# Optimization experiments

Hardware: AMD Instinct MI355X
Metric: run time of the kernel (lower is better)

## Reference

```python
import jax, jax.numpy as jnp
import numpy as np

K_TOKENS = 40  # safety_token_count
LN_EPS = 1e-5


def setup_inputs() -> dict:
    key = jax.random.key(0)
    ks = jax.random.split(key, 3)
    B, S, D = 16, 4096, 768
    H = D // 2
    features = jax.random.normal(ks[0], (B, S, D), dtype=jnp.float32)
    W1 = jax.random.normal(ks[1], (D, H), dtype=jnp.float32) * (1.0 / np.sqrt(D))
    b1 = jnp.zeros((H,), dtype=jnp.float32)
    ln_gamma = jnp.ones((H,), dtype=jnp.float32)
    ln_beta = jnp.zeros((H,), dtype=jnp.float32)
    W2 = jax.random.normal(ks[2], (H, 1), dtype=jnp.float32) * (1.0 / np.sqrt(H))
    b2 = jnp.zeros((1,), dtype=jnp.float32)
    return {"features": features, "W1": W1, "b1": b1,
            "ln_gamma": ln_gamma, "ln_beta": ln_beta, "W2": W2, "b2": b2}


def _scores(features, W1, b1, ln_gamma, ln_beta, W2, b2):
    # Linear -> LayerNorm -> GELU(exact) -> Dropout(eval=identity) -> Linear -> Sigmoid
    h = jnp.einsum('bsd,dh->bsh', features, W1) + b1
    mu = jnp.mean(h, axis=-1, keepdims=True)
    var = jnp.mean(jnp.square(h - mu), axis=-1, keepdims=True)
    h = (h - mu) * jax.lax.rsqrt(var + LN_EPS) * ln_gamma + ln_beta
    h = jax.nn.gelu(h, approximate=False)
    s = jnp.einsum('bsh,ho->bso', h, W2) + b2  # [B, S, 1]
    return jax.nn.sigmoid(s[..., 0])           # [B, S]


def reference(features, W1, b1, ln_gamma, ln_beta, W2, b2):
    scores = _scores(features, W1, b1, ln_gamma, ln_beta, W2, b2)
    k = min(K_TOKENS, features.shape[1])
    _, indices = jax.lax.top_k(scores, k)                      # [B, k]
    safety_tokens = jnp.take_along_axis(features, indices[:, :, None], axis=1)  # [B, k, D]
    return safety_tokens, indices
```

## Files before the change

kernel.cpp:

```cpp
#include <hip/hip_runtime.h>
#include <math.h>

#define B_   16
#define S_   4096
#define D_   768
#define H_   384
#define NTOK (B_ * S_)
#define KTOP 40
#define NTILES 24
#define KCH    24

typedef __attribute__((ext_vector_type(8))) short bf16x8;
typedef __attribute__((ext_vector_type(4))) float f32x4;

static __device__ __forceinline__ unsigned short f2bf(float x) {
    union { float f; unsigned u; } v; v.f = x;
    unsigned r = v.u + 0x7FFF + ((v.u >> 16) & 1);
    return (unsigned short)(r >> 16);
}
static __device__ __forceinline__ float bf2f(unsigned short h) {
    union { unsigned u; float f; } v; v.u = ((unsigned)h) << 16; return v.f;
}

__global__ __launch_bounds__(64) void pack_w1(const float* __restrict__ W1,
                                              unsigned short* __restrict__ bh,
                                              unsigned short* __restrict__ bl)
{
    const int nt   = blockIdx.x;
    const int ch   = blockIdx.y;
    const int lane = threadIdx.x;
    const int n    = nt * 16 + (lane & 15);
    const int k0   = ch * 32 + (lane >> 4) * 8;

    unsigned short h8[8], l8[8];
#pragma unroll
    for (int j = 0; j < 8; ++j) {
        const float v = W1[(size_t)(k0 + j) * H_ + n];
        const unsigned short h = f2bf(v);
        h8[j] = h;
        l8[j] = f2bf(v - bf2f(h));
    }
    const size_t base = ((size_t)(nt * KCH + ch) * 64 + lane) * 8;
#pragma unroll
    for (int j = 0; j < 8; ++j) { bh[base + j] = h8[j]; bl[base + j] = l8[j]; }
}

__global__ __launch_bounds__(256, 3) void score_kernel(
    const float* __restrict__ features,
    const unsigned short* __restrict__ bh_g,
    const unsigned short* __restrict__ bl_g,
    const float* __restrict__ b1,
    const float* __restrict__ gamma,
    const float* __restrict__ beta,
    const float* __restrict__ W2,
    const float* __restrict__ b2,
    float* __restrict__ scores)
{
    __shared__ unsigned short Ah[32][40];
    __shared__ unsigned short Al[32][40];
    __shared__ float red[4][32];
    __shared__ float mu_s[32];
    __shared__ float rs_s[32];

    const int tid  = threadIdx.x;
    const int lane = tid & 63;
    const int w    = tid >> 6;
    const int base = blockIdx.x * 32;
    const int cl   = lane & 15;
    const int p    = lane >> 4;

    f32x4 acc[2][6];
#pragma unroll
    for (int m = 0; m < 2; ++m)
#pragma unroll
        for (int t = 0; t < 6; ++t) acc[m][t] = (f32x4){0.f, 0.f, 0.f, 0.f};

    const int r0 = tid >> 3, c0 = (tid & 7) * 4;

    float4 p0 = *(const float4*)(features + (size_t)(base + r0) * D_ + c0);

    for (int c = 0; c < KCH; ++c) {
        if (c) __syncthreads();
        {
            unsigned short h0 = f2bf(p0.x), h1 = f2bf(p0.y), h2 = f2bf(p0.z), h3 = f2bf(p0.w);
            Ah[r0][c0] = h0; Ah[r0][c0+1] = h1; Ah[r0][c0+2] = h2; Ah[r0][c0+3] = h3;
            Al[r0][c0]   = f2bf(p0.x - bf2f(h0));
            Al[r0][c0+1] = f2bf(p0.y - bf2f(h1));
            Al[r0][c0+2] = f2bf(p0.z - bf2f(h2));
            Al[r0][c0+3] = f2bf(p0.w - bf2f(h3));
        }
        if (c + 1 < KCH) {
            const int d0 = (c + 1) * 32;
            p0 = *(const float4*)(features + (size_t)(base + r0) * D_ + d0 + c0);
        }
        __syncthreads();

        bf16x8 ahf[2], alf[2];
#pragma unroll
        for (int m = 0; m < 2; ++m) {
            const int row = m * 16 + cl;
            const int k0  = p * 8;
            ahf[m] = *(const bf16x8*)&Ah[row][k0];
            alf[m] = *(const bf16x8*)&Al[row][k0];
        }
#pragma unroll
        for (int t = 0; t < 6; ++t) {
            const size_t bb = ((size_t)((w * 6 + t) * KCH + c) * 64 + lane) * 8;
            const bf16x8 bhf = *(const bf16x8*)(bh_g + bb);
            const bf16x8 blf = *(const bf16x8*)(bl_g + bb);
#pragma unroll
            for (int m = 0; m < 2; ++m) {
                acc[m][t] = __builtin_amdgcn_mfma_f32_16x16x32_bf16(ahf[m], bhf, acc[m][t], 0, 0, 0);
                acc[m][t] = __builtin_amdgcn_mfma_f32_16x16x32_bf16(ahf[m], blf, acc[m][t], 0, 0, 0);
                acc[m][t] = __builtin_amdgcn_mfma_f32_16x16x32_bf16(alf[m], bhf, acc[m][t], 0, 0, 0);
            }
        }
    }

    float b1v[6], gv[6], bev[6], w2v[6];
#pragma unroll
    for (int t = 0; t < 6; ++t) {
        const int n = (w * 6 + t) * 16 + cl;
        b1v[t] = b1[n]; gv[t] = gamma[n]; bev[t] = beta[n]; w2v[t] = W2[n];
    }
#pragma unroll
    for (int m = 0; m < 2; ++m)
#pragma unroll
        for (int t = 0; t < 6; ++t)
#pragma unroll
            for (int r = 0; r < 4; ++r) acc[m][t][r] += b1v[t];

#pragma unroll
    for (int m = 0; m < 2; ++m) {
        float sm[4] = {0.f, 0.f, 0.f, 0.f};
#pragma unroll
        for (int t = 0; t < 6; ++t)
#pragma unroll
            for (int r = 0; r < 4; ++r) sm[r] += acc[m][t][r];
#pragma unroll
        for (int r = 0; r < 4; ++r) {
#pragma unroll
            for (int off = 1; off <= 8; off <<= 1) sm[r] += __shfl_xor(sm[r], off, 64);
        }
        if (cl == 0) {
#pragma unroll
            for (int r = 0; r < 4; ++r) red[w][m * 16 + p * 4 + r] = sm[r];
        }
    }
    __syncthreads();
    if (tid < 32) mu_s[tid] = (red[0][tid] + red[1][tid] + red[2][tid] + red[3][tid]) * (1.0f / H_);
    __syncthreads();

#pragma unroll
    for (int m = 0; m < 2; ++m) {
        float mur[4];
#pragma unroll
        for (int r = 0; r < 4; ++r) mur[r] = mu_s[m * 16 + p * 4 + r];
        float sm[4] = {0.f, 0.f, 0.f, 0.f};
#pragma unroll
        for (int t = 0; t < 6; ++t)
#pragma unroll
            for (int r = 0; r < 4; ++r) { const float d = acc[m][t][r] - mur[r]; sm[r] += d * d; }
#pragma unroll
        for (int r = 0; r < 4; ++r) {
#pragma unroll
            for (int off = 1; off <= 8; off <<= 1) sm[r] += __shfl_xor(sm[r], off, 64);
        }
        if (cl == 0) {
#pragma unroll
            for (int r = 0; r < 4; ++r) red[w][m * 16 + p * 4 + r] = sm[r];
        }
    }
    __syncthreads();
    if (tid < 32) rs_s[tid] = rsqrtf((red[0][tid] + red[1][tid] + red[2][tid] + red[3][tid]) * (1.0f / H_) + 1e-5f);
    __syncthreads();

#pragma unroll
    for (int m = 0; m < 2; ++m) {
        float mur[4], rsr[4];
#pragma unroll
        for (int r = 0; r < 4; ++r) { mur[r] = mu_s[m * 16 + p * 4 + r]; rsr[r] = rs_s[m * 16 + p * 4 + r]; }
        float sm[4] = {0.f, 0.f, 0.f, 0.f};
#pragma unroll
        for (int t = 0; t < 6; ++t)
#pragma unroll
            for (int r = 0; r < 4; ++r) {
                const float y  = (acc[m][t][r] - mur[r]) * rsr[r] * gv[t] + bev[t];
                const float ge = 0.5f * y * (1.0f + erff(y * 0.70710678118654752f));
                sm[r] = fmaf(ge, w2v[t], sm[r]);
            }
#pragma unroll
        for (int r = 0; r < 4; ++r) {
#pragma unroll
            for (int off = 1; off <= 8; off <<= 1) sm[r] += __shfl_xor(sm[r], off, 64);
        }
        if (cl == 0) {
#pragma unroll
            for (int r = 0; r < 4; ++r) red[w][m * 16 + p * 4 + r] = sm[r];
        }
    }
    __syncthreads();
    if (tid < 32) {
        const float s = red[0][tid] + red[1][tid] + red[2][tid] + red[3][tid] + b2[0];
        scores[base + tid] = 1.0f / (1.0f + expf(-s));
    }
}

__global__ __launch_bounds__(256) void select_kernel(const float* __restrict__ scores,
                                                     int* __restrict__ sel)
{
    __shared__ unsigned int bits_s[S_];
    __shared__ unsigned int hist[256];
    __shared__ int s_byte, s_above, s_rem;
    __shared__ unsigned int s_ngt, s_neq;
    __shared__ unsigned int candV[64];
    __shared__ int candI[64];
    __shared__ int eqI[256];

    const int b   = blockIdx.x;
    const int tid = threadIdx.x;

    for (int i = tid; i < S_; i += 256)
        bits_s[i] = __float_as_uint(scores[b * S_ + i]);
    if (tid == 0) { s_rem = KTOP; s_ngt = 0u; s_neq = 0u; }

    unsigned int prefix = 0u, mask = 0u;
    for (int pb = 3; pb >= 0; --pb) {
        hist[tid] = 0u;
        __syncthreads();
        for (int i = tid; i < S_; i += 256) {
            const unsigned int u = bits_s[i];
            if ((u & mask) == prefix) atomicAdd(&hist[(u >> (8 * pb)) & 255u], 1u);
        }
        __syncthreads();
        if (tid == 0) {
            int c = 0, v = 255;
            for (; v >= 0; --v) { c += (int)hist[v]; if (c >= s_rem) break; }
            s_byte  = v;
            s_above = c - (int)hist[v];
            s_rem   = s_rem - s_above;
        }
        __syncthreads();
        prefix |= ((unsigned int)s_byte) << (8 * pb);
        mask   |= 0xFFu << (8 * pb);
        __syncthreads();
    }
    const unsigned int T = prefix;
    const int need = s_rem;

    for (int i = tid; i < S_; i += 256) {
        const unsigned int u = bits_s[i];
        if (u > T) {
            const unsigned int pos = atomicAdd(&s_ngt, 1u);
            candV[pos] = u; candI[pos] = i;
        } else if (u == T) {
            const unsigned int pos = atomicAdd(&s_neq, 1u);
            if (pos < 256u) eqI[pos] = i;
        }
    }
    __syncthreads();
    const int ngt = (int)s_ngt;
    const int neq = (int)(s_neq < 256u ? s_neq : 256u);
    for (int j = tid; j < neq; j += 256) {
        int rank = 0;
        for (int l = 0; l < neq; ++l) rank += (eqI[l] < eqI[j]) ? 1 : 0;
        if (rank < need) { candV[ngt + rank] = T; candI[ngt + rank] = eqI[j]; }
    }
    __syncthreads();
    if (tid < KTOP) {
        const unsigned int u = candV[tid];
        const int idx = candI[tid];
        int rank = 0;
        for (int j = 0; j < KTOP; ++j)
            rank += (candV[j] > u || (candV[j] == u && candI[j] < idx)) ? 1 : 0;
        sel[b * KTOP + rank] = idx;
    }
}

__global__ __launch_bounds__(192) void gather_kernel(const float* __restrict__ features,
                                                     const int* __restrict__ sel,
                                                     float* __restrict__ out_tok,
                                                     float* __restrict__ out_idx)
{
    const int i = blockIdx.x;
    const int b = blockIdx.y;
    const int idx = sel[b * KTOP + i];
    const float4* src = (const float4*)(features + ((size_t)b * S_ + idx) * D_);
    float4* dst = (float4*)(out_tok + ((size_t)b * KTOP + i) * D_);
    dst[threadIdx.x] = src[threadIdx.x];
    if (threadIdx.x == 0) out_idx[b * KTOP + i] = (float)idx;
}

extern "C" void kernel_launch(void* const* d_in, const int* in_sizes, int n_in,
                              void* d_out, int out_size, void* d_ws, size_t ws_size,
                              hipStream_t stream)
{
    const float* features = (const float*)d_in[0];
    const float* W1       = (const float*)d_in[1];
    const float* b1       = (const float*)d_in[2];
    const float* gamma    = (const float*)d_in[3];
    const float* beta     = (const float*)d_in[4];
    const float* W2       = (const float*)d_in[5];
    const float* b2       = (const float*)d_in[6];

    unsigned short* bh = (unsigned short*)d_ws;
    unsigned short* bl = bh + (size_t)D_ * H_;
    float* scores      = (float*)(bl + (size_t)D_ * H_);
    int*   sel         = (int*)(scores + NTOK);

    float* out        = (float*)d_out;
    float* out_tokens = out;
    float* out_idx    = out + (size_t)B_ * KTOP * D_;

    pack_w1<<<dim3(NTILES, KCH), 64, 0, stream>>>(W1, bh, bl);
    score_kernel<<<NTOK / 32, 256, 0, stream>>>(features, bh, bl, b1, gamma, beta, W2, b2, scores);
    select_kernel<<<B_, 256, 0, stream>>>(scores, sel);
    gather_kernel<<<dim3(KTOP, B_), 192, 0, stream>>>(features, sel, out_tokens, out_idx);
}
```

Before: 457.0 us.

## Interleave packed W1 hi/lo per lane, raise occupancy, parallelize radix-select scan

Packs W1's bf16 hi and lo halves into one interleaved buffer so each lane reads its six tiles' hi/lo fragments from a single contiguous 192-byte chunk per K-chunk. This replaces two separate strided streams and simplifies address arithmetic. The score kernel's launch bound goes from 3 to 4 blocks per SM, which may pressure registers. The select kernel's serial single-thread histogram walk becomes a wave-shuffle suffix scan, and f2bf now uses the HIP intrinsic.

```diff
diff --git a/kernel.cpp b/kernel.cpp
--- a/kernel.cpp
+++ b/kernel.cpp
@@ -1,4 +1,5 @@
 #include <hip/hip_runtime.h>
+#include <hip/hip_bf16.h>
 #include <math.h>
 
 #define B_   16
@@ -9,46 +10,45 @@
 #define KTOP 40
 #define NTILES 24
 #define KCH    24
+#define CHSTRIDE (4 * 64 * 96)
 
 typedef __attribute__((ext_vector_type(8))) short bf16x8;
 typedef __attribute__((ext_vector_type(4))) float f32x4;
 
 static __device__ __forceinline__ unsigned short f2bf(float x) {
-    union { float f; unsigned u; } v; v.f = x;
-    unsigned r = v.u + 0x7FFF + ((v.u >> 16) & 1);
-    return (unsigned short)(r >> 16);
+    __hip_bfloat16 h = __float2bfloat16(x);
+    unsigned short r;
+    __builtin_memcpy(&r, &h, sizeof(r));
+    return r;
 }
 static __device__ __forceinline__ float bf2f(unsigned short h) {
     union { unsigned u; float f; } v; v.u = ((unsigned)h) << 16; return v.f;
 }
 
 __global__ __launch_bounds__(64) void pack_w1(const float* __restrict__ W1,
-                                              unsigned short* __restrict__ bh,
-                                              unsigned short* __restrict__ bl)
+                                              unsigned short* __restrict__ bp)
 {
     const int nt   = blockIdx.x;
     const int ch   = blockIdx.y;
     const int lane = threadIdx.x;
+    const int w    = nt / 6;
+    const int tl   = nt % 6;
     const int n    = nt * 16 + (lane & 15);
     const int k0   = ch * 32 + (lane >> 4) * 8;
 
-    unsigned short h8[8], l8[8];
+    const size_t dst = ((size_t)(ch * 4 + w) * 64 + lane) * 96 + tl * 16;
 #pragma unroll
     for (int j = 0; j < 8; ++j) {
         const float v = W1[(size_t)(k0 + j) * H_ + n];
         const unsigned short h = f2bf(v);
-        h8[j] = h;
-        l8[j] = f2bf(v - bf2f(h));
-    }
-    const size_t base = ((size_t)(nt * KCH + ch) * 64 + lane) * 8;
-#pragma unroll
-    for (int j = 0; j < 8; ++j) { bh[base + j] = h8[j]; bl[base + j] = l8[j]; }
-}
-
-__global__ __launch_bounds__(256, 3) void score_kernel(
+        bp[dst + j]     = h;
+        bp[dst + 8 + j] = f2bf(v - bf2f(h));
+    }
+}
+
+__global__ __launch_bounds__(256, 4) void score_kernel(
     const float* __restrict__ features,
-    const unsigned short* __restrict__ bh_g,
-    const unsigned short* __restrict__ bl_g,
+    const unsigned short* __restrict__ bp_g,
     const float* __restrict__ b1,
     const float* __restrict__ gamma,
     const float* __restrict__ beta,
@@ -76,8 +76,11 @@
         for (int t = 0; t < 6; ++t) acc[m][t] = (f32x4){0.f, 0.f, 0.f, 0.f};
 
     const int r0 = tid >> 3, c0 = (tid & 7) * 4;
-
-    float4 p0 = *(const float4*)(features + (size_t)(base + r0) * D_ + c0);
+    const float* arow = features + (size_t)(base + r0) * D_ + c0;
+
+    const unsigned short* bpw = bp_g + ((size_t)w * 64 + lane) * 96;
+
+    float4 p0 = *(const float4*)(arow);
 
     for (int c = 0; c < KCH; ++c) {
         if (c) __syncthreads();
@@ -90,8 +93,7 @@
             Al[r0][c0+3] = f2bf(p0.w - bf2f(h3));
         }
         if (c + 1 < KCH) {
-            const int d0 = (c + 1) * 32;
-            p0 = *(const float4*)(features + (size_t)(base + r0) * D_ + d0 + c0);
+            p0 = *(const float4*)(arow + (c + 1) * 32);
         }
         __syncthreads();
 
@@ -99,15 +101,14 @@
 #pragma unroll
         for (int m = 0; m < 2; ++m) {
             const int row = m * 16 + cl;
-            const int k0  = p * 8;
-            ahf[m] = *(const bf16x8*)&Ah[row][k0];
-            alf[m] = *(const bf16x8*)&Al[row][k0];
-        }
+            ahf[m] = *(const bf16x8*)&Ah[row][p * 8];
+            alf[m] = *(const bf16x8*)&Al[row][p * 8];
+        }
+        const unsigned short* bb = bpw + (size_t)c * CHSTRIDE;
 #pragma unroll
         for (int t = 0; t < 6; ++t) {
-            const size_t bb = ((size_t)((w * 6 + t) * KCH + c) * 64 + lane) * 8;
-            const bf16x8 bhf = *(const bf16x8*)(bh_g + bb);
-            const bf16x8 blf = *(const bf16x8*)(bl_g + bb);
+            const bf16x8 bhf = *(const bf16x8*)(bb + t * 16);
+            const bf16x8 blf = *(const bf16x8*)(bb + t * 16 + 8);
 #pragma unroll
             for (int m = 0; m < 2; ++m) {
                 acc[m][t] = __builtin_amdgcn_mfma_f32_16x16x32_bf16(ahf[m], bhf, acc[m][t], 0, 0, 0);
@@ -211,14 +212,18 @@
 {
     __shared__ unsigned int bits_s[S_];
     __shared__ unsigned int hist[256];
-    __shared__ int s_byte, s_above, s_rem;
+    __shared__ unsigned int suf[256];
+    __shared__ unsigned int wtot[4];
+    __shared__ int s_byte, s_rem;
     __shared__ unsigned int s_ngt, s_neq;
     __shared__ unsigned int candV[64];
     __shared__ int candI[64];
     __shared__ int eqI[256];
 
-    const int b   = blockIdx.x;
-    const int tid = threadIdx.x;
+    const int b    = blockIdx.x;
+    const int tid  = threadIdx.x;
+    const int lane = tid & 63;
+    const int w4   = tid >> 6;
 
     for (int i = tid; i < S_; i += 256)
         bits_s[i] = __float_as_uint(scores[b * S_ + i]);
@@ -233,12 +238,27 @@
             if ((u & mask) == prefix) atomicAdd(&hist[(u >> (8 * pb)) & 255u], 1u);
         }
         __syncthreads();
-        if (tid == 0) {
-            int c = 0, v = 255;
-            for (; v >= 0; --v) { c += (int)hist[v]; if (c >= s_rem) break; }
-            s_byte  = v;
-            s_above = c - (int)hist[v];
-            s_rem   = s_rem - s_above;
+        {
+            unsigned int v = hist[tid];
+#pragma unroll
+            for (int off = 1; off < 64; off <<= 1) {
+                const unsigned int y = __shfl_down(v, off, 64);
+                if (lane + off < 64) v += y;
+            }
+            if (lane == 0) wtot[w4] = v;
+            __syncthreads();
+            unsigned int add = 0u;
+#pragma unroll
+            for (int j = 0; j < 4; ++j) if (j > w4) add += wtot[j];
+            v += add;
+            suf[tid] = v;
+            __syncthreads();
+            const int rem = s_rem;
+            const unsigned int nxt = (tid < 255) ? suf[tid + 1] : 0u;
+            if (suf[tid] >= (unsigned)rem && (tid == 255 || nxt < (unsigned)rem)) {
+                s_byte = tid;
+                s_rem  = rem - (int)nxt;
+            }
         }
         __syncthreads();
         prefix |= ((unsigned int)s_byte) << (8 * pb);
@@ -303,17 +323,16 @@
     const float* W2       = (const float*)d_in[5];
     const float* b2       = (const float*)d_in[6];
 
-    unsigned short* bh = (unsigned short*)d_ws;
-    unsigned short* bl = bh + (size_t)D_ * H_;
-    float* scores      = (float*)(bl + (size_t)D_ * H_);
+    unsigned short* bp = (unsigned short*)d_ws;
+    float* scores      = (float*)(bp + (size_t)2 * D_ * H_);
     int*   sel         = (int*)(scores + NTOK);
 
     float* out        = (float*)d_out;
     float* out_tokens = out;
     float* out_idx    = out + (size_t)B_ * KTOP * D_;
 
-    pack_w1<<<dim3(NTILES, KCH), 64, 0, stream>>>(W1, bh, bl);
-    score_kernel<<<NTOK / 32, 256, 0, stream>>>(features, bh, bl, b1, gamma, beta, W2, b2, scores);
+    pack_w1<<<dim3(NTILES, KCH), 64, 0, stream>>>(W1, bp);
+    score_kernel<<<NTOK / 32, 256, 0, stream>>>(features, bp, b1, gamma, beta, W2, b2, scores);
     select_kernel<<<B_, 256, 0, stream>>>(scores, sel);
     gather_kernel<<<dim3(KTOP, B_), 192, 0, stream>>>(features, sel, out_tokens, out_idx);
 }
```

Result: slower. 491.0 us (+7.4%).
